# Kernel tuning notes

Measured on AMD Instinct MI355X. Metric: run time of the kernel, lower is better.

The kernel has to match this reference:

```python
import jax, jax.numpy as jnp
import numpy as np

NUM_HEADS = 8
WIN = (7, 7)


def _window_setup(H, W, hw, ww):
    # replicates idx_map_pad / token_window / nearest-interpolated window_map
    pad_h = (hw - H % hw) % hw
    pad_w = (ww - W % ww) % ww
    H_pad, W_pad = H + pad_h, W + pad_w
    nh, nw = H_pad // hw, W_pad // ww
    idx_map = jnp.arange(H * W, dtype=jnp.int32).reshape(H, W)
    idx_map_pad = jnp.full((H_pad, W_pad), H * W, dtype=jnp.int32)
    idx_map_pad = idx_map_pad.at[pad_h // 2:pad_h // 2 + H, pad_w // 2:pad_w // 2 + W].set(idx_map)
    token_window = idx_map_pad.reshape(nh, hw, nw, ww).transpose(0, 2, 1, 3).reshape(nh * nw, hw * ww)
    # nearest upsample of arange(nh*nw).reshape(nh,nw) to (H_pad,W_pad) then crop:
    # H_pad divisible by hw, so nearest index = padded_coord // hw
    ys = (jnp.arange(H, dtype=jnp.int32) + pad_h // 2) // hw
    xs = (jnp.arange(W, dtype=jnp.int32) + pad_w // 2) // ww
    window_map = ys[:, None] * nw + xs[None, :]  # [H, W]
    return token_window, window_map, nh * nw


def _grid_idx(loc_orig, H, W, dtype):
    xy = 0.5 * (loc_orig + 1.0) * jnp.array([W, H], dtype=dtype) - 0.5
    xg = jnp.clip(jnp.round(xy[..., 0]).astype(jnp.int32), 0, W - 1)
    yg = jnp.clip(jnp.round(xy[..., 1]).astype(jnp.int32), 0, H - 1)
    return xg, yg


def _token2map(feat, loc_orig, idx_agg_src, H, W):
    # scatter-average token features onto the H*W grid. feat: [B,Ns,Cp] -> [B,H*W,Cp]
    B, N0 = idx_agg_src.shape
    xg, yg = _grid_idx(jax.lax.stop_gradient(loc_orig), H, W, feat.dtype)
    pix = yg * W + xg  # [B, N0]
    f0 = jnp.take_along_axis(feat, idx_agg_src[..., None], axis=1)  # [B,N0,Cp]
    bidx = jnp.broadcast_to(jnp.arange(B, dtype=jnp.int32)[:, None], (B, N0))
    mp = jnp.zeros((B, H * W, feat.shape[-1]), feat.dtype).at[bidx, pix].add(f0)
    cnt = jnp.zeros((B, H * W, 1), feat.dtype).at[bidx, pix].add(1.0)
    return mp / (cnt + 1e-6)


def _forward(x, loc_orig, idx_agg, agg_weight, x_source, idx_agg_source, conf_source,
             H, W, q_w, q_b, kv_w, kv_b, proj_w, proj_b):
    B, N, C = x.shape
    Ns = x_source.shape[1]
    N0 = idx_agg_source.shape[1]
    Hh = NUM_HEADS
    d = C // Hh
    scale = d ** -0.5
    hw, ww = WIN
    token_window, window_map, nWin = _window_setup(H, W, hw, ww)  # [nWin,K], [H,W]

    q = (x @ q_w + q_b).reshape(B, N, Hh, d).transpose(0, 2, 1, 3)  # [B,Hh,N,d]

    # --- window assignment (no-grad block in torch) ---
    if H * W == N and Ns == N and N == N0:
        idx_window = jnp.broadcast_to(window_map.reshape(1, N), (B, N))
    else:
        lo = jax.lax.stop_gradient(loc_orig)
        xg, yg = _grid_idx(lo, H, W, x.dtype)
        idx_tmp = window_map[yg, xg]  # [B,N0] window id per original position
        bidx = jnp.broadcast_to(jnp.arange(B, dtype=jnp.int32)[:, None], (B, N0))
        pw = jnp.zeros((B, N, nWin), x.dtype).at[bidx, idx_agg, idx_tmp].add(
            jax.lax.stop_gradient(agg_weight).reshape(B, N0))
        idx_window = jnp.argmax(pw, axis=-1)  # [B,N]
    idx_K = token_window[idx_window]  # [B,N,K] key-pixel ids (H*W == pad token)

    # --- token2map: rasterize source tokens (+conf) onto grid ---
    src = jnp.concatenate([x_source, conf_source], axis=-1)  # [B,Ns,C+1]
    smap = _token2map(src, loc_orig, idx_agg_source, H, W)  # [B,H*W,C+1]
    xs = smap[..., :C]
    cs = smap[..., C:]
    xs = jnp.concatenate([xs, jnp.zeros((B, 1, C), xs.dtype)], axis=1)  # pad token
    cs = jnp.concatenate([cs, jnp.full((B, 1, 1), -jnp.inf, cs.dtype)], axis=1)

    M = H * W + 1
    kv = (xs @ kv_w + kv_b).reshape(B, M, 2, Hh, d).transpose(2, 0, 3, 1, 4)
    k, v = kv[0], kv[1]  # [B,Hh,M,d]

    # gather K/V per query window (f_attn / f_weighted_sum)
    kg = jax.vmap(lambda kb, ib: kb[:, ib])(k, idx_K)  # [B,Hh,N,K,d]
    vg = jax.vmap(lambda vb, ib: vb[:, ib])(v, idx_K)  # [B,Hh,N,K,d]
    conf_g = jax.vmap(lambda cb, ib: cb[ib, 0])(cs, idx_K)  # [B,N,K]

    attn = jnp.einsum('bhnd,bhnkd->bhnk', q * scale, kg) + conf_g[:, None]
    attn = jax.nn.softmax(attn, axis=-1)
    out = jnp.einsum('bhnk,bhnkd->bhnd', attn, vg)
    out = out.transpose(0, 2, 1, 3).reshape(B, N, C)
    return out @ proj_w + proj_b


def setup_inputs() -> dict:
    key = jax.random.key(0)
    ks = jax.random.split(key, 10)
    B, N, C, N0, H, W = 4, 784, 384, 3136, 56, 56
    x = jax.random.normal(ks[0], (B, N, C), jnp.float32)
    loc_orig = jax.random.uniform(ks[1], (B, N0, 2), jnp.float32, -1.0, 1.0)
    idx_agg = jax.random.randint(ks[2], (B, N0), 0, N, dtype=jnp.int32)
    agg_weight = jax.random.uniform(ks[3], (B, N0, 1), jnp.float32)
    x_source = jax.random.normal(ks[4], (B, N, C), jnp.float32)
    idx_agg_source = jax.random.randint(ks[5], (B, N0), 0, N, dtype=jnp.int32)
    conf_source = jax.random.normal(ks[6], (B, N, 1), jnp.float32)
    q_w = jax.random.normal(ks[7], (C, C), jnp.float32) * 0.02
    q_b = jnp.zeros((C,), jnp.float32)
    kv_w = jax.random.normal(ks[8], (C, 2 * C), jnp.float32) * 0.02
    kv_b = jnp.zeros((2 * C,), jnp.float32)
    proj_w = jax.random.normal(ks[9], (C, C), jnp.float32) * 0.02
    proj_b = jnp.zeros((C,), jnp.float32)
    return {'x': x, 'loc_orig': loc_orig, 'idx_agg': idx_agg, 'agg_weight': agg_weight,
            'x_source': x_source, 'idx_agg_source': idx_agg_source, 'conf_source': conf_source,
            'H': H, 'W': W, 'q_w': q_w, 'q_b': q_b, 'kv_w': kv_w, 'kv_b': kv_b,
            'proj_w': proj_w, 'proj_b': proj_b}


def reference(x, loc_orig, idx_agg, agg_weight, x_source, idx_agg_source, conf_source,
              H, W, q_w, q_b, kv_w, kv_b, proj_w, proj_b):
    return _forward(x, loc_orig, idx_agg, agg_weight, x_source, idx_agg_source, conf_source,
                    H, W, q_w, q_b, kv_w, kv_b, proj_w, proj_b)
```

## Files before the change

kernel.cpp:

```cpp
#include <hip/hip_runtime.h>
#include <hip/hip_bf16.h>
#include <cstdint>
#include <type_traits>

constexpr int B    = 4;
constexpr int N    = 784;
constexpr int C    = 384;
constexpr int NH   = 8;
constexpr int D    = 48;
constexpr int Himg = 56;
constexpr int Wimg = 56;
constexpr int HW   = 3136;
constexpr int NSRC = 3136;
constexpr int NWIN = 64;
constexpr int KWIN = 49;
constexpr int KPAD = 56;
constexpr int C2   = 2 * C;
constexpr int CAP  = 24;

constexpr size_t OFF_PW      = 0;
constexpr size_t SZ_PW       = (size_t)B * N * NWIN;
constexpr size_t OFF_CSUM    = OFF_PW + SZ_PW;
constexpr size_t SZ_CSUM     = (size_t)B * HW;
constexpr size_t OFF_CNT     = OFF_CSUM + SZ_CSUM;
constexpr size_t SZ_CNT      = (size_t)B * HW;
constexpr size_t ZERO_FLOATS = OFF_CNT + SZ_CNT;
constexpr size_t OFF_SLOTS   = ZERO_FLOATS;
constexpr size_t SZ_SLOTS    = (size_t)B * HW * CAP;
constexpr size_t OFF_Q       = OFF_SLOTS + SZ_SLOTS;
constexpr size_t SZ_Q        = (size_t)B * N * C;
constexpr size_t OFF_IDXW    = OFF_Q + SZ_Q;
constexpr size_t SZ_IDXW     = (size_t)B * N;
constexpr size_t OFF_ATTNO   = OFF_IDXW + SZ_IDXW;
constexpr size_t SZ_ATTNO_F  = ((size_t)B * N * C + 1) / 2;
constexpr size_t OFF_KV_F    = OFF_ATTNO + SZ_ATTNO_F;
constexpr size_t SZ_KV_F     = ((size_t)B * HW * C2 + 1) / 2;
constexpr size_t OFF_ABF_F   = OFF_KV_F + SZ_KV_F;
constexpr size_t SZ_ABF_F    = ((size_t)B * HW * C + 1) / 2;
constexpr size_t MAIN_BYTES  = (OFF_ABF_F + SZ_ABF_F) * 4;
constexpr size_t OFF_KVWT_BYTE  = MAIN_BYTES;
constexpr size_t SZ_KVWT        = (size_t)C2 * C;
constexpr size_t OFF_QWT_BYTE   = OFF_KVWT_BYTE + SZ_KVWT * 2;
constexpr size_t SZ_QWT         = (size_t)C * C;
constexpr size_t OFF_PROJWT_BYTE= OFF_QWT_BYTE + SZ_QWT * 2;
constexpr size_t SZ_PROJWT      = (size_t)C * C;
constexpr size_t OFF_FLAG_BYTE  = OFF_PROJWT_BYTE + SZ_PROJWT * 2;
constexpr size_t OFF_XBF_BYTE   = OFF_FLAG_BYTE + 16;
constexpr size_t SZ_XBF         = (size_t)B * N * C;
constexpr size_t WS_BYTES_NEEDED = OFF_XBF_BYTE + SZ_XBF * 2;

typedef __attribute__((ext_vector_type(8))) short bf16x8;
typedef __attribute__((ext_vector_type(8))) unsigned short u16x8;
typedef __attribute__((ext_vector_type(4))) float f32x4;

__device__ __forceinline__ unsigned short f2bf_bits(float f) {
    __hip_bfloat16 h = __float2bfloat16(f);
    return *reinterpret_cast<unsigned short*>(&h);
}
__device__ __forceinline__ float bflo(unsigned w) { return __uint_as_float(w << 16); }
__device__ __forceinline__ float bfhi(unsigned w) { return __uint_as_float(w & 0xffff0000u); }
__device__ __forceinline__ float bfbits2f(unsigned short u) {
    return __uint_as_float(((unsigned)u) << 16);
}

__device__ __forceinline__ float ldin(const void* p, size_t i, bool f32) {
    if (f32) return ((const float*)p)[i];
    return __bfloat162float(((const __hip_bfloat16*)p)[i]);
}

__device__ __forceinline__ void grid_idx(float lx, float ly, int& xg, int& yg) {
    float xf = 0.5f * (lx + 1.0f) * (float)Wimg - 0.5f;
    float yf = 0.5f * (ly + 1.0f) * (float)Himg - 0.5f;
    int x = (int)rintf(xf);
    int y = (int)rintf(yf);
    xg = min(max(x, 0), Wimg - 1);
    yg = min(max(y, 0), Himg - 1);
}

__global__ __launch_bounds__(64) void sniff_kernel(const unsigned short* __restrict__ qw_bits,
                                                   int* __restrict__ flag) {
    int t = threadIdx.x;
    int cnt = 0;
    #pragma unroll
    for (int i = 0; i < 8; i++) {
        unsigned u = qw_bits[t * 8 + i];
        float v = __uint_as_float(u << 16);
        if (fabsf(v) > 4.0f) cnt++;
    }
    #pragma unroll
    for (int off = 32; off >= 1; off >>= 1) cnt += __shfl_xor(cnt, off);
    if (t == 0) *flag = (cnt > 8) ? 1 : 0;
}

__device__ __forceinline__ void do_transpose_tile(
    const void* __restrict__ W, unsigned short* __restrict__ Wt,
    int K, int Nn, int n0, int k0, bool f32, int t, float (*tile)[33])
{
    int tx = t & 31, ty = t >> 5;
    #pragma unroll
    for (int i = 0; i < 4; i++)
        tile[ty + i * 8][tx] = ldin(W, (size_t)(k0 + ty + i * 8) * Nn + (n0 + tx), f32);
    __syncthreads();
    #pragma unroll
    for (int i = 0; i < 4; i++)
        Wt[(size_t)(n0 + ty + i * 8) * K + (k0 + tx)] = f2bf_bits(tile[tx][ty + i * 8]);
}

constexpr int PREP_BLOCKS = 1801;
__global__ __launch_bounds__(256) void prep_kernel(
    const void* __restrict__ kv_w, unsigned short* __restrict__ kvwt,
    const void* __restrict__ q_w, unsigned short* __restrict__ qwt,
    const void* __restrict__ proj_w, unsigned short* __restrict__ projwt,
    const void* __restrict__ x, unsigned short* __restrict__ xbf,
    const void* __restrict__ loc, const int* __restrict__ idx_agg,
    const void* __restrict__ agg_w, const int* __restrict__ idx_agg_src,
    const void* __restrict__ conf_src,
    float* __restrict__ pw, float* __restrict__ csum, int* __restrict__ cnti,
    int* __restrict__ slots, const int* __restrict__ flagp)
{
    __shared__ float tile[32][33];
    const bool f32 = (*flagp != 0);
    const int bid = blockIdx.x, t = threadIdx.x;
    if (bid < 288) {
        int j = bid;
        do_transpose_tile(kv_w, kvwt, C, C2, (j % 24) * 32, (j / 24) * 32, f32, t, tile);
    } else if (bid < 432) {
        int j = bid - 288;
        do_transpose_tile(q_w, qwt, C, C, (j % 12) * 32, (j / 12) * 32, f32, t, tile);
    } else if (bid < 576) {
        int j = bid - 432;
        do_transpose_tile(proj_w, projwt, C, C, (j % 12) * 32, (j / 12) * 32, f32, t, tile);
    } else if (bid < 1752) {
        int i = (bid - 576) * 1024 + t * 4;
        #pragma unroll
        for (int j = 0; j < 4; j++)
            xbf[i + j] = f2bf_bits(ldin(x, i + j, f32));
    } else {
        int p = (bid - 1752) * 256 + t;
        if (p < B * NSRC) {
            int b = p / NSRC;
            float lx = ldin(loc, (size_t)p * 2 + 0, f32);
            float ly = ldin(loc, (size_t)p * 2 + 1, f32);
            int xg, yg; grid_idx(lx, ly, xg, yg);
            int pix = yg * Wimg + xg;
            size_t bp = (size_t)b * HW + pix;
            int s = idx_agg_src[p];
            int slot = atomicAdd(&cnti[bp], 1);
            if (slot < CAP) slots[bp * CAP + slot] = s;
            atomicAdd(&csum[bp], ldin(conf_src, (size_t)b * N + s, f32));
            int win = (yg / 7) * 8 + (xg / 7);
            int n = idx_agg[p];
            atomicAdd(&pw[((size_t)b * N + n) * NWIN + win], ldin(agg_w, p, f32));
        }
    }
}

__global__ __launch_bounds__(256) void gather_kernel(
    const void* __restrict__ x_source,
    const int* __restrict__ cnti, const int* __restrict__ slots,
    unsigned short* __restrict__ abf, const int* __restrict__ flagp)
{
    const bool f32 = (*flagp != 0);
    const int g = blockIdx.x * 4 + (threadIdx.x >> 6);
    const int lane = threadIdx.x & 63;
    const int cf = cnti[g];
    const float sc = 1.0f / ((float)cf + 1e-6f);
    const int cn = min(cf, CAP);
    const int bb = g / HW;
    float a[6] = {0.f, 0.f, 0.f, 0.f, 0.f, 0.f};
    for (int si = 0; si < cn; si++) {
        int src = slots[(size_t)g * CAP + si];
        size_t off = ((size_t)bb * N + src) * C + lane * 6;
        if (f32) {
            const float* xr = (const float*)x_source + off;
            #pragma unroll
            for (int e = 0; e < 6; e++) a[e] += xr[e];
        } else {
            const unsigned short* xr = (const unsigned short*)x_source + off;
            #pragma unroll
            for (int e = 0; e < 6; e++) a[e] += bfbits2f(xr[e]);
        }
    }
    unsigned short* dst = abf + (size_t)g * C + lane * 6;
    unsigned w0 = (unsigned)f2bf_bits(a[0] * sc) | ((unsigned)f2bf_bits(a[1] * sc) << 16);
    unsigned w1 = (unsigned)f2bf_bits(a[2] * sc) | ((unsigned)f2bf_bits(a[3] * sc) << 16);
    unsigned w2 = (unsigned)f2bf_bits(a[4] * sc) | ((unsigned)f2bf_bits(a[5] * sc) << 16);
    ((unsigned*)dst)[0] = w0;
    ((unsigned*)dst)[1] = w1;
    ((unsigned*)dst)[2] = w2;
}

constexpr int KV_RT   = (B * HW) / 64;
constexpr int KV_CT   = C2 / 128;
constexpr int KV_SPAN = 200;
constexpr int KV_REGION = KV_CT * KV_SPAN;
constexpr int Q_RT    = (B * N) / 64;
constexpr int Q_CT    = C / 128;
constexpr int Q_SPAN  = 56;
constexpr int Q_REGION = Q_CT * Q_SPAN;
constexpr int AM_BLOCKS = (B * N + 255) / 256;
constexpr int MID_BLOCKS = KV_REGION + Q_REGION + AM_BLOCKS;
__global__ __launch_bounds__(256) void mid_kernel(
    const unsigned short* __restrict__ abf,
    const unsigned short* __restrict__ kvwt, const void* __restrict__ kv_b,
    unsigned short* __restrict__ kv_out,
    const unsigned short* __restrict__ xbf, const unsigned short* __restrict__ qwt,
    const void* __restrict__ q_b, float* __restrict__ q_out,
    const float* __restrict__ pw, int* __restrict__ idxw,
    const int* __restrict__ flagp, float scale)
{
    constexpr int SA = 40;
    __shared__ unsigned short As[64 * SA];
    __shared__ unsigned short Bs[128 * SA];
    const bool f32 = (*flagp != 0);
    const int bid = blockIdx.x;
    const int t = threadIdx.x;

    if (bid >= KV_REGION + Q_REGION) {
        int tt = (bid - KV_REGION - Q_REGION) * 256 + t;
        if (tt < B * N) {
            const float* row = pw + (size_t)tt * NWIN;
            float best = row[0]; int bi = 0;
            for (int j = 1; j < NWIN; j++) {
                float v = row[j];
                if (v > best) { best = v; bi = j; }
            }
            idxw[tt] = bi;
        }
        return;
    }

    bool iskv; int R, sct;
    if (bid < KV_REGION) {
        iskv = true;  sct = bid / KV_SPAN; R = bid % KV_SPAN;
        if (R >= KV_RT) return;
    } else {
        iskv = false; int b2 = bid - KV_REGION; sct = b2 / Q_SPAN; R = b2 % Q_SPAN;
        if (R >= Q_RT) return;
    }
    const int bm = R * 64, bn = sct * 128;
    const int M  = iskv ? B * HW : B * N;
    const int Nn = iskv ? C2 : C;
    const int K  = C;
    const unsigned short* A  = iskv ? abf : xbf;
    const unsigned short* Bt = iskv ? kvwt : qwt;
    const void* bias = iskv ? kv_b : q_b;
    const float alpha = iskv ? 1.0f : scale;

    const int wave = t >> 6, lane = t & 63;
    const int quad = lane >> 4, l16 = lane & 15;
    const int wm = (wave >> 1) * 32, wn = (wave & 1) * 64;

    f32x4 acc[2][4] = {};

    for (int k0 = 0; k0 < K; k0 += 32) {
        {
            int row = t >> 2, ch = t & 3;
            int grow = bm + row; if (grow >= M) grow = M - 1;
            *(u16x8*)&As[row * SA + ch * 8] =
                *(const u16x8*)(A + (size_t)grow * K + k0 + ch * 8);
        }
        #pragma unroll
        for (int ss = 0; ss < 2; ss++) {
            int sI = t + ss * 256;
            int row = sI >> 2, ch = sI & 3;
            *(u16x8*)&Bs[row * SA + ch * 8] =
                *(const u16x8*)(Bt + (size_t)(bn + row) * K + k0 + ch * 8);
        }
        __syncthreads();

        bf16x8 af[2], bf[4];
        #pragma unroll
        for (int i = 0; i < 2; i++)
            af[i] = *(const bf16x8*)&As[(wm + i * 16 + l16) * SA + quad * 8];
        #pragma unroll
        for (int j = 0; j < 4; j++)
            bf[j] = *(const bf16x8*)&Bs[(wn + j * 16 + l16) * SA + quad * 8];
        #pragma unroll
        for (int i = 0; i < 2; i++)
            #pragma unroll
            for (int jj = 0; jj < 4; jj++)
                acc[i][jj] = __builtin_amdgcn_mfma_f32_16x16x32_bf16(af[i], bf[jj], acc[i][jj], 0, 0, 0);
        __syncthreads();
    }

    #pragma unroll
    for (int i = 0; i < 2; i++) {
        int growb = bm + wm + i * 16 + quad * 4;
        #pragma unroll
        for (int jj = 0; jj < 4; jj++) {
            int gcol = bn + wn + jj * 16 + l16;
            float bv = ldin(bias, gcol, f32);
            #pragma unroll
            for (int r = 0; r < 4; r++) {
                int grow = growb + r;
                if (grow < M) {
                    float v = (acc[i][jj][r] + bv) * alpha;
                    size_t idx = (size_t)grow * Nn + gcol;
                    if (iskv) kv_out[idx] = f2bf_bits(v);
                    else      q_out[idx] = v;
                }
            }
        }
    }
}

__global__ __launch_bounds__(256) void mfma_gemm_kernel(
    const unsigned short* __restrict__ A,
    const unsigned short* __restrict__ Bt,
    const void* __restrict__ bias,
    void* __restrict__ Co,
    int M, int Nn, int K, float alpha, const int* __restrict__ flagp)
{
    constexpr int SA = 40;
    const bool f32 = (*flagp != 0);
    __shared__ unsigned short As[128 * SA];
    __shared__ unsigned short Bs[128 * SA];
    const int t = threadIdx.x;
    const int wave = t >> 6, lane = t & 63;
    const int quad = lane >> 4, l16 = lane & 15;
    const int wm = (wave >> 1) * 64, wn = (wave & 1) * 64;
    const int bm = blockIdx.y * 128, bn = blockIdx.x * 128;

    f32x4 acc[4][4] = {};

    for (int k0 = 0; k0 < K; k0 += 32) {
        #pragma unroll
        for (int ss = 0; ss < 2; ss++) {
            int s = t + ss * 256;
            int row = s >> 2, ch = s & 3;
            int grow = bm + row; if (grow >= M) grow = M - 1;
            *(u16x8*)&As[row * SA + ch * 8] =
                *(const u16x8*)(A + (size_t)grow * K + k0 + ch * 8);
            *(u16x8*)&Bs[row * SA + ch * 8] =
                *(const u16x8*)(Bt + (size_t)(bn + row) * K + k0 + ch * 8);
        }
        __syncthreads();

        bf16x8 af[4], bf[4];
        #pragma unroll
        for (int i = 0; i < 4; i++) {
            af[i] = *(const bf16x8*)&As[(wm + i * 16 + l16) * SA + quad * 8];
            bf[i] = *(const bf16x8*)&Bs[(wn + i * 16 + l16) * SA + quad * 8];
        }
        #pragma unroll
        for (int i = 0; i < 4; i++)
            #pragma unroll
            for (int j = 0; j < 4; j++)
                acc[i][j] = __builtin_amdgcn_mfma_f32_16x16x32_bf16(af[i], bf[j], acc[i][j], 0, 0, 0);
        __syncthreads();
    }

    #pragma unroll
    for (int i = 0; i < 4; i++) {
        int growb = bm + wm + i * 16 + quad * 4;
        #pragma unroll
        for (int j = 0; j < 4; j++) {
            int gcol = bn + wn + j * 16 + l16;
            float bv = ldin(bias, gcol, f32);
            #pragma unroll
            for (int r = 0; r < 4; r++) {
                int grow = growb + r;
                if (grow < M) {
                    float v = (acc[i][j][r] + bv) * alpha;
                    size_t idx = (size_t)grow * Nn + gcol;
                    if (f32) ((float*)Co)[idx] = v;
                    else     ((unsigned short*)Co)[idx] = f2bf_bits(v);
                }
            }
        }
    }
}

__global__ __launch_bounds__(512, 4) void attn_win_kernel(
    const float* __restrict__ q,
    const unsigned short* __restrict__ kv,
    const float* __restrict__ csum,
    const int* __restrict__ cnti,
    const int* __restrict__ idxw,
    unsigned short* __restrict__ attno)
{
    constexpr int SK  = 104;
    constexpr int SVT = 58;
    constexpr int CH  = 2 * D;
    __shared__ unsigned short s_k[KWIN * SK];
    __shared__ unsigned short s_vt[CH * SVT];
    __shared__ float s_p[8][KPAD];
    __shared__ unsigned short s_list[N];
    __shared__ float s_conf[KWIN];
    __shared__ int   s_cnt;

    const int t   = threadIdx.x;
    const int blk = blockIdx.x;
    const int b   = blk >> 8;
    const int win = (blk >> 2) & 63;
    const int par = blk & 3;
    const int wy = win >> 3, wx = win & 7;

    if (t == 0) s_cnt = 0;
    __syncthreads();
    for (int n = t; n < N; n += 512) {
        if (idxw[b * N + n] == win) {
            int slot = atomicAdd(&s_cnt, 1);
            s_list[slot] = (unsigned short)n;
        }
    }
    const unsigned* kvw = (const unsigned*)kv;
    for (int idx = t; idx < KWIN * (CH / 2); idx += 512) {
        int row = idx / (CH / 2), cw = idx % (CH / 2);
        int pix = (wy * 7 + row / 7) * Wimg + wx * 7 + row % 7;
        size_t gbase = ((size_t)b * HW + pix) * 384 + par * (CH / 2);
        *(unsigned*)&s_k[row * SK + cw * 2] = kvw[gbase + cw];
        unsigned vv = kvw[gbase + 192 + cw];
        int c0 = cw * 2;
        s_vt[(c0 + 0) * SVT + row] = (unsigned short)(vv & 0xffffu);
        s_vt[(c0 + 1) * SVT + row] = (unsigned short)(vv >> 16);
    }
    if (t < CH) {
        #pragma unroll
        for (int j = KWIN; j < KPAD; j++) s_vt[t * SVT + j] = 0;
    }
    if (t < KWIN) {
        int pix = (wy * 7 + t / 7) * Wimg + wx * 7 + t % 7;
        size_t bp = (size_t)b * HW + pix;
        s_conf[t] = csum[bp] / ((float)cnti[bp] + 1e-6f);
    }
    __syncthreads();

    const int cnt   = s_cnt;
    const int wave  = t >> 6;
    const int lane  = t & 63;
    const int hloc  = __builtin_amdgcn_readfirstlane(wave & 1);
    const int quart = wave >> 1;
    const int h     = par * 2 + hloc;

    if (lane >= KWIN && lane < KPAD) s_p[wave][lane] = 0.0f;

    const int krow = (lane < KWIN) ? lane : 0;
    uint4 kf[3];
    #pragma unroll
    for (int j = 0; j < 3; j++)
        kf[j] = *(const uint4*)&s_k[krow * SK + hloc * D + j * 16];
    const int dl = (lane < D) ? lane : 0;
    unsigned vw[28];
    {
        const unsigned short* vrow = &s_vt[(hloc * D + dl) * SVT];
        #pragma unroll
        for (int j = 0; j < 28; j++) vw[j] = *(const unsigned*)&vrow[j * 2];
    }
    const float confk = (lane < KWIN) ? s_conf[lane] : 0.0f;

    for (int ti = quart; ti < cnt; ti += 4) {
        const int n0 = __builtin_amdgcn_readfirstlane((int)s_list[ti]);
        const size_t bn = (size_t)b * N + n0;
        const float* qrow = q + bn * C + h * D;

        float l = -INFINITY;
        if (lane < KWIN) {
            float acc = confk;
            #pragma unroll
            for (int j = 0; j < 3; j++) {
                const int c = j * 16;
                acc += qrow[c +  0] * bflo(kf[j].x) + qrow[c +  1] * bfhi(kf[j].x);
                acc += qrow[c +  2] * bflo(kf[j].y) + qrow[c +  3] * bfhi(kf[j].y);
                acc += qrow[c +  4] * bflo(kf[j].z) + qrow[c +  5] * bfhi(kf[j].z);
                acc += qrow[c +  6] * bflo(kf[j].w) + qrow[c +  7] * bfhi(kf[j].w);
                uint4 k2 = *(const uint4*)&s_k[krow * SK + hloc * D + j * 16 + 8];
                acc += qrow[c +  8] * bflo(k2.x) + qrow[c +  9] * bfhi(k2.x);
                acc += qrow[c + 10] * bflo(k2.y) + qrow[c + 11] * bfhi(k2.y);
                acc += qrow[c + 12] * bflo(k2.z) + qrow[c + 13] * bfhi(k2.z);
                acc += qrow[c + 14] * bflo(k2.w) + qrow[c + 15] * bfhi(k2.w);
            }
            l = acc;
        }
        float m = l;
        #pragma unroll
        for (int off = 32; off >= 1; off >>= 1) m = fmaxf(m, __shfl_xor(m, off));
        float e = (lane < KWIN) ? expf(l - m) : 0.0f;
        float ssum = e;
        #pragma unroll
        for (int off = 32; off >= 1; off >>= 1) ssum += __shfl_xor(ssum, off);
        if (lane < KWIN) s_p[wave][lane] = e / ssum;
        __builtin_amdgcn_wave_barrier();

        float acc = 0.0f;
        const float4* pv4 = (const float4*)&s_p[wave][0];
        #pragma unroll
        for (int j = 0; j < KPAD / 4; j++) {
            float4 p4 = pv4[j];
            unsigned w0 = vw[j * 2], w1 = vw[j * 2 + 1];
            acc += p4.x * bflo(w0) + p4.y * bfhi(w0);
            acc += p4.z * bflo(w1) + p4.w * bfhi(w1);
        }
        if (lane < D) attno[bn * C + h * D + lane] = f2bf_bits(acc);
    }
}

extern "C" void kernel_launch(void* const* d_in, const int* in_sizes, int n_in,
                              void* d_out, int out_size, void* d_ws, size_t ws_size,
                              hipStream_t stream) {
    if (ws_size < WS_BYTES_NEEDED) return;

    const void* x        = d_in[0];
    const void* loc      = d_in[1];
    const int*  idx_agg  = (const int*)d_in[2];
    const void* agg_w    = d_in[3];
    const void* x_source = d_in[4];
    const int*  idx_asrc = (const int*)d_in[5];
    const void* conf_src = d_in[6];
    int wb = 9;
    if (!(n_in >= 15 && in_sizes[7] == 1 && in_sizes[8] == 1)) wb = 7;
    const void* q_w    = d_in[wb + 0];
    const void* q_b    = d_in[wb + 1];
    const void* kv_w   = d_in[wb + 2];
    const void* kv_b   = d_in[wb + 3];
    const void* proj_w = d_in[wb + 4];
    const void* proj_b = d_in[wb + 5];

    float* ws   = (float*)d_ws;
    float* pw   = ws + OFF_PW;
    float* csum = ws + OFF_CSUM;
    int*   cnti = (int*)(ws + OFF_CNT);
    int*   slots = (int*)(ws + OFF_SLOTS);
    float* q    = ws + OFF_Q;
    int*   idxw = (int*)(ws + OFF_IDXW);
    unsigned short* attno = (unsigned short*)(ws + OFF_ATTNO);
    unsigned short* kv  = (unsigned short*)(ws + OFF_KV_F);
    unsigned short* abf = (unsigned short*)(ws + OFF_ABF_F);
    unsigned short* kvwt   = (unsigned short*)((char*)d_ws + OFF_KVWT_BYTE);
    unsigned short* qwt    = (unsigned short*)((char*)d_ws + OFF_QWT_BYTE);
    unsigned short* projwt = (unsigned short*)((char*)d_ws + OFF_PROJWT_BYTE);
    int* flag = (int*)((char*)d_ws + OFF_FLAG_BYTE);
    unsigned short* xbf = (unsigned short*)((char*)d_ws + OFF_XBF_BYTE);

    sniff_kernel<<<1, 64, 0, stream>>>((const unsigned short*)q_w, flag);
    hipMemsetAsync(ws, 0, ZERO_FLOATS * sizeof(float), stream);
    prep_kernel<<<PREP_BLOCKS, 256, 0, stream>>>(
        kv_w, kvwt, q_w, qwt, proj_w, projwt, x, xbf,
        loc, idx_agg, agg_w, idx_asrc, conf_src,
        pw, csum, cnti, slots, flag);
    gather_kernel<<<B * HW / 4, 256, 0, stream>>>(x_source, cnti, slots, abf, flag);
    const float scale = (float)(1.0 / sqrt((double)D));
    mid_kernel<<<MID_BLOCKS, 256, 0, stream>>>(
        abf, kvwt, kv_b, kv, xbf, qwt, q_b, q, pw, idxw, flag, scale);
    attn_win_kernel<<<B * NWIN * 4, 512, 0, stream>>>(q, kv, csum, cnti, idxw, attno);
    mfma_gemm_kernel<<<dim3(C / 128, (B * N + 127) / 128), 256, 0, stream>>>(
        attno, projwt, proj_b, d_out, B * N, C, C, 1.0f, flag);

    (void)out_size;
}
```

Before: 186.4 us.

## Use direct global-to-LDS loads in GEMMs and fuse memset into sniff kernel

GEMM tile staging now uses global_load_lds, which copies 16 bytes per lane straight into shared memory without passing through registers. The LDS row stride drops from the padded 40 to an unpadded 32, which may cause bank conflicts when the MFMA fragments are read. The mid kernel also drops its row-bound clamps and store guards, relying on M being a multiple of 64. The separate sniff kernel and memset are merged into one init kernel, removing a launch.

```diff
diff --git a/kernel.cpp b/kernel.cpp
--- a/kernel.cpp
+++ b/kernel.cpp
@@ -63,6 +63,12 @@
     return __uint_as_float(((unsigned)u) << 16);
 }
 
+__device__ __forceinline__ void gl_lds16(const unsigned short* g, unsigned short* l) {
+    __builtin_amdgcn_global_load_lds(
+        (const __attribute__((address_space(1))) void*)g,
+        (__attribute__((address_space(3))) void*)l, 16, 0, 0);
+}
+
 __device__ __forceinline__ float ldin(const void* p, size_t i, bool f32) {
     if (f32) return ((const float*)p)[i];
     return __bfloat162float(((const __hip_bfloat16*)p)[i]);
@@ -77,19 +83,32 @@
     yg = min(max(y, 0), Himg - 1);
 }
 
-__global__ __launch_bounds__(64) void sniff_kernel(const unsigned short* __restrict__ qw_bits,
-                                                   int* __restrict__ flag) {
-    int t = threadIdx.x;
-    int cnt = 0;
-    #pragma unroll
-    for (int i = 0; i < 8; i++) {
-        unsigned u = qw_bits[t * 8 + i];
-        float v = __uint_as_float(u << 16);
-        if (fabsf(v) > 4.0f) cnt++;
-    }
-    #pragma unroll
-    for (int off = 32; off >= 1; off >>= 1) cnt += __shfl_xor(cnt, off);
-    if (t == 0) *flag = (cnt > 8) ? 1 : 0;
+constexpr int INIT_BLOCKS = 222;
+__global__ __launch_bounds__(256) void init_kernel(
+    const unsigned short* __restrict__ qw_bits, int* __restrict__ flag,
+    float* __restrict__ zbase)
+{
+    const int bid = blockIdx.x, t = threadIdx.x;
+    if (bid == 0) {
+        if (t < 64) {
+            int cnt = 0;
+            #pragma unroll
+            for (int i = 0; i < 8; i++) {
+                unsigned u = qw_bits[t * 8 + i];
+                float v = __uint_as_float(u << 16);
+                if (fabsf(v) > 4.0f) cnt++;
+            }
+            #pragma unroll
+            for (int off = 32; off >= 1; off >>= 1) cnt += __shfl_xor(cnt, off);
+            if (t == 0) *flag = (cnt > 8) ? 1 : 0;
+        }
+    } else {
+        size_t i = (size_t)(bid - 1) * 1024 + t * 4;
+        if (i + 3 < ZERO_FLOATS)
+            *(float4*)&zbase[i] = float4{0.f, 0.f, 0.f, 0.f};
+        else
+            for (size_t j = i; j < ZERO_FLOATS; j++) zbase[j] = 0.f;
+    }
 }
 
 __device__ __forceinline__ void do_transpose_tile(
@@ -209,9 +228,8 @@
     const float* __restrict__ pw, int* __restrict__ idxw,
     const int* __restrict__ flagp, float scale)
 {
-    constexpr int SA = 40;
-    __shared__ unsigned short As[64 * SA];
-    __shared__ unsigned short Bs[128 * SA];
+    __shared__ unsigned short As[64 * 32];
+    __shared__ unsigned short Bs[128 * 32];
     const bool f32 = (*flagp != 0);
     const int bid = blockIdx.x;
     const int t = threadIdx.x;
@@ -239,7 +257,6 @@
         if (R >= Q_RT) return;
     }
     const int bm = R * 64, bn = sct * 128;
-    const int M  = iskv ? B * HW : B * N;
     const int Nn = iskv ? C2 : C;
     const int K  = C;
     const unsigned short* A  = iskv ? abf : xbf;
@@ -250,32 +267,30 @@
     const int wave = t >> 6, lane = t & 63;
     const int quad = lane >> 4, l16 = lane & 15;
     const int wm = (wave >> 1) * 32, wn = (wave & 1) * 64;
+    const int srow = lane >> 2;
+    const int sch  = (lane & 3) * 8;
 
     f32x4 acc[2][4] = {};
 
     for (int k0 = 0; k0 < K; k0 += 32) {
         {
-            int row = t >> 2, ch = t & 3;
-            int grow = bm + row; if (grow >= M) grow = M - 1;
-            *(u16x8*)&As[row * SA + ch * 8] =
-                *(const u16x8*)(A + (size_t)grow * K + k0 + ch * 8);
-        }
-        #pragma unroll
-        for (int ss = 0; ss < 2; ss++) {
-            int sI = t + ss * 256;
-            int row = sI >> 2, ch = sI & 3;
-            *(u16x8*)&Bs[row * SA + ch * 8] =
-                *(const u16x8*)(Bt + (size_t)(bn + row) * K + k0 + ch * 8);
+            int ar = wave * 16 + srow;
+            gl_lds16(A + (size_t)(bm + ar) * K + k0 + sch, &As[ar * 32 + sch]);
+        }
+        #pragma unroll
+        for (int c2 = 0; c2 < 2; c2++) {
+            int br = wave * 32 + c2 * 16 + srow;
+            gl_lds16(Bt + (size_t)(bn + br) * K + k0 + sch, &Bs[br * 32 + sch]);
         }
         __syncthreads();
 
         bf16x8 af[2], bf[4];
         #pragma unroll
         for (int i = 0; i < 2; i++)
-            af[i] = *(const bf16x8*)&As[(wm + i * 16 + l16) * SA + quad * 8];
+            af[i] = *(const bf16x8*)&As[(wm + i * 16 + l16) * 32 + quad * 8];
         #pragma unroll
         for (int j = 0; j < 4; j++)
-            bf[j] = *(const bf16x8*)&Bs[(wn + j * 16 + l16) * SA + quad * 8];
+            bf[j] = *(const bf16x8*)&Bs[(wn + j * 16 + l16) * 32 + quad * 8];
         #pragma unroll
         for (int i = 0; i < 2; i++)
             #pragma unroll
@@ -293,13 +308,10 @@
             float bv = ldin(bias, gcol, f32);
             #pragma unroll
             for (int r = 0; r < 4; r++) {
-                int grow = growb + r;
-                if (grow < M) {
-                    float v = (acc[i][jj][r] + bv) * alpha;
-                    size_t idx = (size_t)grow * Nn + gcol;
-                    if (iskv) kv_out[idx] = f2bf_bits(v);
-                    else      q_out[idx] = v;
-                }
+                float v = (acc[i][jj][r] + bv) * alpha;
+                size_t idx = (size_t)(growb + r) * Nn + gcol;
+                if (iskv) kv_out[idx] = f2bf_bits(v);
+                else      q_out[idx] = v;
             }
         }
     }
@@ -312,36 +324,34 @@
     void* __restrict__ Co,
     int M, int Nn, int K, float alpha, const int* __restrict__ flagp)
 {
-    constexpr int SA = 40;
     const bool f32 = (*flagp != 0);
-    __shared__ unsigned short As[128 * SA];
-    __shared__ unsigned short Bs[128 * SA];
+    __shared__ unsigned short As[128 * 32];
+    __shared__ unsigned short Bs[128 * 32];
     const int t = threadIdx.x;
     const int wave = t >> 6, lane = t & 63;
     const int quad = lane >> 4, l16 = lane & 15;
     const int wm = (wave >> 1) * 64, wn = (wave & 1) * 64;
     const int bm = blockIdx.y * 128, bn = blockIdx.x * 128;
+    const int srow = lane >> 2;
+    const int sch  = (lane & 3) * 8;
 
     f32x4 acc[4][4] = {};
 
     for (int k0 = 0; k0 < K; k0 += 32) {
         #pragma unroll
-        for (int ss = 0; ss < 2; ss++) {
-            int s = t + ss * 256;
-            int row = s >> 2, ch = s & 3;
-            int grow = bm + row; if (grow >= M) grow = M - 1;
-            *(u16x8*)&As[row * SA + ch * 8] =
-                *(const u16x8*)(A + (size_t)grow * K + k0 + ch * 8);
-            *(u16x8*)&Bs[row * SA + ch * 8] =
-                *(const u16x8*)(Bt + (size_t)(bn + row) * K + k0 + ch * 8);
+        for (int c2 = 0; c2 < 2; c2++) {
+            int ar = wave * 32 + c2 * 16 + srow;
+            int grow = bm + ar; if (grow >= M) grow = M - 1;
+            gl_lds16(A + (size_t)grow * K + k0 + sch, &As[ar * 32 + sch]);
+            gl_lds16(Bt + (size_t)(bn + ar) * K + k0 + sch, &Bs[ar * 32 + sch]);
         }
         __syncthreads();
 
         bf16x8 af[4], bf[4];
         #pragma unroll
         for (int i = 0; i < 4; i++) {
-            af[i] = *(const bf16x8*)&As[(wm + i * 16 + l16) * SA + quad * 8];
-            bf[i] = *(const bf16x8*)&Bs[(wn + i * 16 + l16) * SA + quad * 8];
+            af[i] = *(const bf16x8*)&As[(wm + i * 16 + l16) * 32 + quad * 8];
+            bf[i] = *(const bf16x8*)&Bs[(wn + i * 16 + l16) * 32 + quad * 8];
         }
         #pragma unroll
         for (int i = 0; i < 4; i++)
@@ -533,8 +543,7 @@
     int* flag = (int*)((char*)d_ws + OFF_FLAG_BYTE);
     unsigned short* xbf = (unsigned short*)((char*)d_ws + OFF_XBF_BYTE);
 
-    sniff_kernel<<<1, 64, 0, stream>>>((const unsigned short*)q_w, flag);
-    hipMemsetAsync(ws, 0, ZERO_FLOATS * sizeof(float), stream);
+    init_kernel<<<INIT_BLOCKS, 256, 0, stream>>>((const unsigned short*)q_w, flag, ws);
     prep_kernel<<<PREP_BLOCKS, 256, 0, stream>>>(
         kv_w, kvwt, q_w, qwt, proj_w, projwt, x, xbf,
         loc, idx_agg, agg_w, idx_asrc, conf_src,
```

Result: faster. 179.5 us (-3.7%).
